# Performance work log

Measured on AMD Instinct MI355X. Metric: run time of the kernel, lower is better.

## Reference

```python
import jax, jax.numpy as jnp
import numpy as np

LOG_STD_MAX = 2.0
LOG_STD_MIN = -5.0
N_LAYERS = 10
HID = 512
OBS = 21
ACT = 8
OVERALL = HID * (N_LAYERS + 1)          # 5632
IN_DIM = OBS + OVERALL                   # 5653
OUT_DIM = OVERALL + ACT                  # 5640
BATCH = 8192


def _block_banded_weight(rng):
    # staircase partitions, exactly as layer_init
    in_d = [0, OBS] + [OBS + HID * i for i in range(1, N_LAYERS + 2)]
    out_d = [0] + [HID * i for i in range(1, N_LAYERS + 2)] + [OUT_DIM]
    W = np.zeros((OUT_DIM, IN_DIM), dtype=np.float32)
    for i in range(N_LAYERS + 2):
        r0, r1 = out_d[i], out_d[i + 1]
        c0, c1 = in_d[i], in_d[i + 1]
        fan_in = c1 - c0
        std = np.sqrt(2.0 / fan_in)  # kaiming_normal_ fan_in, gain sqrt(2)
        W[r0:r1, c0:c1] = rng.standard_normal((r1 - r0, c1 - c0)).astype(np.float32) * std
    return jnp.asarray(W)


def setup_inputs() -> dict:
    key = jax.random.key(0)
    k1, k2, k3, k4, k5, k6 = jax.random.split(key, 6)
    rng = np.random.default_rng(0)
    return {
        "obs": jax.random.normal(k1, (BATCH, OBS), dtype=jnp.float32),
        "hidden0": jax.random.uniform(k2, (BATCH, OVERALL), dtype=jnp.float32),
        "prev_mean": jax.random.normal(k3, (BATCH, ACT), dtype=jnp.float32),
        "prev_logstd": jax.random.normal(k4, (BATCH, ACT), dtype=jnp.float32),
        "W_mean": _block_banded_weight(rng),
        "b_mean": jnp.zeros((OUT_DIM,), dtype=jnp.float32),
        "W_logstd": jax.random.normal(k5, (ACT, IN_DIM), dtype=jnp.float32) / np.sqrt(IN_DIM),
        "b_logstd": jax.random.normal(k6, (ACT,), dtype=jnp.float32) * 0.01,
    }


def reference(obs, hidden0, prev_mean, prev_logstd, W_mean, b_mean, W_logstd, b_logstd):
    x = jnp.concatenate([obs, hidden0], axis=1)            # [B, IN_DIM]
    new_x = x @ W_mean.T + b_mean                          # [B, OUT_DIM]
    new_hidden = jax.nn.relu(new_x[:, :-ACT])              # [B, OVERALL]
    new_mean = new_x[:, -ACT:]                             # [B, ACT]
    new_log_std = x @ W_logstd.T + b_logstd                # [B, ACT]
    # outputs come from the PREVIOUS step's (mean, log_std)
    log_std = jnp.tanh(prev_logstd)
    log_std = LOG_STD_MIN + 0.5 * (LOG_STD_MAX - LOG_STD_MIN) * (log_std + 1.0)
    return (prev_mean, log_std, new_hidden, new_mean, new_log_std)
```

## Files before the change

kernel.cpp:

```cpp
#include <hip/hip_runtime.h>
#include <math.h>

typedef unsigned short u16;
typedef unsigned int u32;
typedef __attribute__((ext_vector_type(8))) short short8;
typedef __attribute__((ext_vector_type(4))) float float4v;

#define BATCH   8192
#define OBS     21
#define HID     512
#define NL      10
#define OVERALL 5632
#define IN_DIM  5653
#define ACT     8

#define O_PM   0
#define O_LS   65536
#define O_NH   131072
#define O_NM   (131072 + BATCH*OVERALL)
#define O_NLS  (O_NM + 65536)

#define WSP_TOTAL (10*512*512)
#define WSP_BYTES ((size_t)WSP_TOTAL * 2)

__device__ __forceinline__ u16 f2bf(float f) {
    u32 u = __float_as_uint(f);
    u32 r = (u + 0x7fffu + ((u >> 16) & 1u)) >> 16;
    return (u16)r;
}
__device__ __forceinline__ u32 pkbf(float a, float b) {
    return (u32)f2bf(a) | ((u32)f2bf(b) << 16);
}
__device__ __forceinline__ void gload_lds16(const void* g, void* l) {
    __builtin_amdgcn_global_load_lds(
        (const __attribute__((address_space(1))) char*)g,
        (__attribute__((address_space(3))) char*)l, 16, 0, 0);
}

__global__ __launch_bounds__(256) void k_pack(const float* __restrict__ Wm,
                                              u16* __restrict__ ws) {
    int idx = blockIdx.x * 256 + threadIdx.x;
    if (idx >= WSP_TOTAL) return;
    int z = idx >> 18;
    int rem = idx & 262143;
    int n = rem >> 9, k = rem & 511;
    float v = Wm[(size_t)(512 * (z + 1) + n) * IN_DIM + OBS + 512 * z + k];
    ws[idx] = f2bf(v);
}

#define BM 128
#define BK 32
#define LDA 40
__global__ __launch_bounds__(1024, 4) void k_fused(
        const float* __restrict__ X,
        const float* __restrict__ Wm_raw,
        const u16* __restrict__ Wp,
        const float* __restrict__ Wls_raw,
        const float* __restrict__ b_mean,
        float* __restrict__ out_h,
        float* __restrict__ out_ls,
        float* __restrict__ out_mean,
        int packed) {
    __shared__ __attribute__((aligned(16))) u16 As[BM * LDA];
    __shared__ __attribute__((aligned(16))) u16 Bs[512 * 32];
    __shared__ __attribute__((aligned(16))) u16 Wt[16 * 520];
    u16* Wt2 = (u16*)Bs;

    int t = threadIdx.x;
    int w = t >> 6, lane = t & 63;
    int quad = lane >> 4, r16 = lane & 15;
    int gm = blockIdx.x * BM;
    int z = blockIdx.y;
    bool mainz = (z < 10);
    int wm = (w >> 3) * 64;
    int wn = (w & 7) * 64;

    {
        int n = t >> 7;
        int k4 = (t & 127) * 4;
        const float* wr = Wls_raw + (size_t)n * IN_DIM + OBS + z * 512 + k4;
        u16* dst = &Wt[n * 520 + k4];
        dst[0] = f2bf(wr[0]); dst[1] = f2bf(wr[1]);
        dst[2] = f2bf(wr[2]); dst[3] = f2bf(wr[3]);
        if (!mainz) {
            const float* wr2 = Wm_raw + (size_t)(OVERALL + n) * IN_DIM + OBS + z * 512 + k4;
            u16* d2 = &Wt2[n * 520 + k4];
            d2[0] = f2bf(wr2[0]); d2[1] = f2bf(wr2[1]);
            d2[2] = f2bf(wr2[2]); d2[3] = f2bf(wr2[3]);
        }
    }

    int arow = t >> 3;
    int acol = (t & 7) * 4;
    const float* gA = X + (size_t)(gm + arow) * OVERALL + (size_t)z * 512 + acol;
    float4 areg = *(const float4*)(gA);

    float4v acc[4][4];
#pragma unroll
    for (int i = 0; i < 4; i++)
#pragma unroll
        for (int j = 0; j < 4; j++) acc[i][j] = (float4v)0.f;
    float4v accL = (float4v)0.f;

    for (int it = 0; it < 16; ++it) {
        int k0 = it * BK;
        __syncthreads();
        {
            uint2 p;
            p.x = pkbf(areg.x, areg.y);
            p.y = pkbf(areg.z, areg.w);
            *(uint2*)&As[arow * LDA + acol] = p;
        }
        if (mainz) {
            if (packed) {
#pragma unroll
                for (int i2 = 0; i2 < 2; ++i2) {
                    int base_row = i2 * 256 + w * 16;
                    int row = base_row + (lane >> 2);
                    int slot = lane & 3;
                    int j = (slot - row) & 3;
                    const u16* g = Wp + (size_t)z * 262144 + (size_t)row * 512 + k0 + j * 8;
                    gload_lds16(g, (char*)Bs + base_row * 64);
                }
            } else {
#pragma unroll
                for (int i2 = 0; i2 < 2; ++i2) {
                    int row = i2 * 256 + w * 16 + (lane >> 2);
                    int slot = lane & 3;
                    int j = (slot - row) & 3;
                    const float* g = Wm_raw + (size_t)(512 * (z + 1) + row) * IN_DIM
                                     + OBS + (size_t)z * 512 + k0 + j * 8;
                    uint4 q;
                    q.x = pkbf(g[0], g[1]); q.y = pkbf(g[2], g[3]);
                    q.z = pkbf(g[4], g[5]); q.w = pkbf(g[6], g[7]);
                    *(uint4*)&Bs[row * 32 + slot * 8] = q;
                }
            }
        }
        __syncthreads();
        if (it < 15) areg = *(const float4*)(gA + (it + 1) * BK);

        if (mainz) {
            short8 bfr[4];
#pragma unroll
            for (int j = 0; j < 4; j++) {
                int n = wn + j * 16 + r16;
                int s = (quad + n) & 3;
                bfr[j] = *(const short8*)&Bs[n * 32 + s * 8];
            }
#pragma unroll
            for (int i2 = 0; i2 < 4; i2++) {
                short8 af = *(const short8*)&As[(wm + i2 * 16 + r16) * LDA + quad * 8];
#pragma unroll
                for (int j = 0; j < 4; j++)
                    acc[i2][j] = __builtin_amdgcn_mfma_f32_16x16x32_bf16(af, bfr[j], acc[i2][j], 0, 0, 0);
            }
        }
        if (w < 8) {
            short8 aL = *(const short8*)&As[(w * 16 + r16) * LDA + quad * 8];
            short8 bL = *(const short8*)&Wt[r16 * 520 + k0 + quad * 8];
            accL = __builtin_amdgcn_mfma_f32_16x16x32_bf16(aL, bL, accL, 0, 0, 0);
        } else if (!mainz) {
            short8 aL = *(const short8*)&As[((w - 8) * 16 + r16) * LDA + quad * 8];
            short8 bL = *(const short8*)&Wt2[r16 * 520 + k0 + quad * 8];
            accL = __builtin_amdgcn_mfma_f32_16x16x32_bf16(aL, bL, accL, 0, 0, 0);
        }
    }

    if (mainz) {
        int colblock = (z + 1) * 512;
#pragma unroll
        for (int j = 0; j < 4; j++) {
            int n_loc = wn + j * 16 + r16;
            float bias = b_mean[colblock + n_loc];
#pragma unroll
            for (int i2 = 0; i2 < 4; i2++) {
                int m0 = gm + wm + i2 * 16 + quad * 4;
#pragma unroll
                for (int r = 0; r < 4; r++) {
                    float v = acc[i2][j][r] + bias;
                    out_h[(size_t)(m0 + r) * OVERALL + colblock + n_loc] = fmaxf(v, 0.f);
                }
            }
        }
    }
    if (w < 8) {
        if (r16 < ACT) {
#pragma unroll
            for (int r = 0; r < 4; r++) {
                int row = gm + w * 16 + quad * 4 + r;
                atomicAdd(&out_ls[(size_t)row * ACT + r16], accL[r]);
            }
        }
    } else if (!mainz) {
        if (r16 < ACT) {
            float bias = b_mean[OVERALL + r16];
#pragma unroll
            for (int r = 0; r < 4; r++) {
                int row = gm + (w - 8) * 16 + quad * 4 + r;
                out_mean[(size_t)row * ACT + r16] = accL[r] + bias;
            }
        }
    }
}

#define B0_ROWS 32
__global__ __launch_bounds__(256) void k_block0(const float* __restrict__ obs,
                                                const float* __restrict__ Wm,
                                                const float* __restrict__ b_mean,
                                                float* __restrict__ out_h) {
    __shared__ float w0[OBS * 512];
    __shared__ float bias_s[512];
    __shared__ float obs_s[B0_ROWS * OBS];
    int t = threadIdx.x;
    int b0 = blockIdx.x * B0_ROWS;
    for (int i = t; i < OBS * 512; i += 256) {
        int n = i / OBS, k = i - n * OBS;
        w0[k * 512 + n] = Wm[(size_t)n * IN_DIM + k];
    }
    for (int i = t; i < 512; i += 256) bias_s[i] = b_mean[i];
    for (int i = t; i < B0_ROWS * OBS; i += 256) obs_s[i] = obs[(size_t)b0 * OBS + i];
    __syncthreads();

    int n0 = (t & 127) * 4;
    int rh = t >> 7;
#pragma unroll 4
    for (int r = 0; r < 16; r++) {
        int row = rh * 16 + r;
        float acc0 = bias_s[n0], acc1 = bias_s[n0 + 1];
        float acc2 = bias_s[n0 + 2], acc3 = bias_s[n0 + 3];
#pragma unroll
        for (int k = 0; k < OBS; k++) {
            float xo = obs_s[row * OBS + k];
            const float* wr = &w0[k * 512 + n0];
            acc0 += xo * wr[0]; acc1 += xo * wr[1];
            acc2 += xo * wr[2]; acc3 += xo * wr[3];
        }
        float4 o;
        o.x = fmaxf(acc0, 0.f); o.y = fmaxf(acc1, 0.f);
        o.z = fmaxf(acc2, 0.f); o.w = fmaxf(acc3, 0.f);
        *(float4*)&out_h[(size_t)(b0 + row) * OVERALL + n0] = o;
    }
}

__global__ __launch_bounds__(256) void k_finish(const float* __restrict__ obs,
                                                const float* __restrict__ Wls,
                                                const float* __restrict__ b_logstd,
                                                const float* __restrict__ pm,
                                                const float* __restrict__ pls,
                                                float* __restrict__ o_pm,
                                                float* __restrict__ o_lstd,
                                                float* __restrict__ o_nls) {
    __shared__ float wobs[ACT * OBS];
    __shared__ float bls[ACT];
    int t = threadIdx.x;
    if (t < ACT * OBS) wobs[t] = Wls[(size_t)(t / OBS) * IN_DIM + (t % OBS)];
    if (t < ACT) bls[t] = b_logstd[t];
    __syncthreads();
    int row = blockIdx.x * 256 + t;
    float ob[OBS];
#pragma unroll
    for (int k = 0; k < OBS; k++) ob[k] = obs[(size_t)row * OBS + k];
#pragma unroll
    for (int n = 0; n < ACT; n++) {
        float a = bls[n];
#pragma unroll
        for (int k = 0; k < OBS; k++) a += ob[k] * wobs[n * OBS + k];
        o_nls[(size_t)row * ACT + n] += a;
    }
    float4 p0 = *(const float4*)(pm + (size_t)row * ACT);
    float4 p1 = *(const float4*)(pm + (size_t)row * ACT + 4);
    *(float4*)(o_pm + (size_t)row * ACT) = p0;
    *(float4*)(o_pm + (size_t)row * ACT + 4) = p1;
    float4 l0 = *(const float4*)(pls + (size_t)row * ACT);
    float4 l1 = *(const float4*)(pls + (size_t)row * ACT + 4);
    float4 q0, q1;
    q0.x = -5.f + 3.5f * (tanhf(l0.x) + 1.f);
    q0.y = -5.f + 3.5f * (tanhf(l0.y) + 1.f);
    q0.z = -5.f + 3.5f * (tanhf(l0.z) + 1.f);
    q0.w = -5.f + 3.5f * (tanhf(l0.w) + 1.f);
    q1.x = -5.f + 3.5f * (tanhf(l1.x) + 1.f);
    q1.y = -5.f + 3.5f * (tanhf(l1.y) + 1.f);
    q1.z = -5.f + 3.5f * (tanhf(l1.z) + 1.f);
    q1.w = -5.f + 3.5f * (tanhf(l1.w) + 1.f);
    *(float4*)(o_lstd + (size_t)row * ACT) = q0;
    *(float4*)(o_lstd + (size_t)row * ACT + 4) = q1;
}

extern "C" void kernel_launch(void* const* d_in, const int* in_sizes, int n_in,
                              void* d_out, int out_size, void* d_ws, size_t ws_size,
                              hipStream_t stream) {
    const float* obs         = (const float*)d_in[0];
    const float* hidden0     = (const float*)d_in[1];
    const float* prev_mean   = (const float*)d_in[2];
    const float* prev_logstd = (const float*)d_in[3];
    const float* W_mean      = (const float*)d_in[4];
    const float* b_mean      = (const float*)d_in[5];
    const float* W_logstd    = (const float*)d_in[6];
    const float* b_logstd    = (const float*)d_in[7];

    float* out   = (float*)d_out;
    float* o_pm  = out + O_PM;
    float* o_ls  = out + O_LS;
    float* o_nh  = out + O_NH;
    float* o_nm  = out + O_NM;
    float* o_nls = out + O_NLS;
    u16*   ws    = (u16*)d_ws;

    int packed = (ws != nullptr && ws_size >= WSP_BYTES) ? 1 : 0;

    if (packed) {
        k_pack<<<(WSP_TOTAL + 255) / 256, 256, 0, stream>>>(W_mean, ws);
    }
    hipMemsetAsync(o_nls, 0, (size_t)BATCH * ACT * sizeof(float), stream);
    k_fused<<<dim3(BATCH / BM, NL + 1), 1024, 0, stream>>>(
        hidden0, W_mean, ws, W_logstd, b_mean, o_nh, o_nls, o_nm, packed);
    k_block0<<<BATCH / B0_ROWS, 256, 0, stream>>>(obs, W_mean, b_mean, o_nh);
    k_finish<<<BATCH / 256, 256, 0, stream>>>(obs, W_logstd, b_logstd,
                                              prev_mean, prev_logstd,
                                              o_pm, o_ls, o_nls);
}
```

Measured before the change: 453.8 us.

## Split fused GEMM blocks into four 256-thread column quarters

Each diagonal block's 512-column output is now split across four smaller workgroups of 256 threads instead of one 1024-thread workgroup, with vectorized 16-wide fp32-to-bf16 conversion for A and the head weights. The goal is more, smaller workgroups for better occupancy and scheduling. The trade-off is that each A tile is read and converted four times, raising global or cache traffic. The B LDS swizzle is also dropped, which may introduce bank conflicts.

```diff
diff --git a/kernel.cpp b/kernel.cpp
--- a/kernel.cpp
+++ b/kernel.cpp
@@ -35,6 +35,19 @@
     __builtin_amdgcn_global_load_lds(
         (const __attribute__((address_space(1))) char*)g,
         (__attribute__((address_space(3))) char*)l, 16, 0, 0);
+}
+__device__ __forceinline__ void cvt16(const float* __restrict__ g, u16* dst) {
+    float4 f0 = *(const float4*)(g);
+    float4 f1 = *(const float4*)(g + 4);
+    float4 f2 = *(const float4*)(g + 8);
+    float4 f3 = *(const float4*)(g + 12);
+    uint4 q0, q1;
+    q0.x = pkbf(f0.x, f0.y); q0.y = pkbf(f0.z, f0.w);
+    q0.z = pkbf(f1.x, f1.y); q0.w = pkbf(f1.z, f1.w);
+    q1.x = pkbf(f2.x, f2.y); q1.y = pkbf(f2.z, f2.w);
+    q1.z = pkbf(f3.x, f3.y); q1.w = pkbf(f3.z, f3.w);
+    *(uint4*)dst = q0;
+    *(uint4*)(dst + 8) = q1;
 }
 
 __global__ __launch_bounds__(256) void k_pack(const float* __restrict__ Wm,
@@ -51,7 +64,7 @@
 #define BM 128
 #define BK 32
 #define LDA 40
-__global__ __launch_bounds__(1024, 4) void k_fused(
+__global__ __launch_bounds__(256, 3) void k_fused(
         const float* __restrict__ X,
         const float* __restrict__ Wm_raw,
         const u16* __restrict__ Wp,
@@ -62,91 +75,97 @@
         float* __restrict__ out_mean,
         int packed) {
     __shared__ __attribute__((aligned(16))) u16 As[BM * LDA];
-    __shared__ __attribute__((aligned(16))) u16 Bs[512 * 32];
-    __shared__ __attribute__((aligned(16))) u16 Wt[16 * 520];
-    u16* Wt2 = (u16*)Bs;
-
-    int t = threadIdx.x;
-    int w = t >> 6, lane = t & 63;
-    int quad = lane >> 4, r16 = lane & 15;
-    int gm = blockIdx.x * BM;
-    int z = blockIdx.y;
-    bool mainz = (z < 10);
-    int wm = (w >> 3) * 64;
-    int wn = (w & 7) * 64;
-
-    {
-        int n = t >> 7;
-        int k4 = (t & 127) * 4;
-        const float* wr = Wls_raw + (size_t)n * IN_DIM + OBS + z * 512 + k4;
-        u16* dst = &Wt[n * 520 + k4];
-        dst[0] = f2bf(wr[0]); dst[1] = f2bf(wr[1]);
-        dst[2] = f2bf(wr[2]); dst[3] = f2bf(wr[3]);
-        if (!mainz) {
-            const float* wr2 = Wm_raw + (size_t)(OVERALL + n) * IN_DIM + OBS + z * 512 + k4;
-            u16* d2 = &Wt2[n * 520 + k4];
-            d2[0] = f2bf(wr2[0]); d2[1] = f2bf(wr2[1]);
-            d2[2] = f2bf(wr2[2]); d2[3] = f2bf(wr2[3]);
-        }
-    }
-
-    int arow = t >> 3;
-    int acol = (t & 7) * 4;
-    const float* gA = X + (size_t)(gm + arow) * OVERALL + (size_t)z * 512 + acol;
-    float4 areg = *(const float4*)(gA);
+    __shared__ __attribute__((aligned(16))) u16 Bs[128 * 32];
+    __shared__ __attribute__((aligned(16))) u16 Wt[8 * 520];
+    __shared__ __attribute__((aligned(16))) u16 Wt2[8 * 520];
+
+    const int t = threadIdx.x;
+    const int w = t >> 6, lane = t & 63;
+    const int quad = lane >> 4, r16 = lane & 15;
+    const int gm = blockIdx.x * BM;
+    const int y = blockIdx.y;
+    const bool mainz = (y < 40);
+    const int z = mainz ? (y >> 2) : 10;
+    const int h = y & 3;
+    const bool do_ls = (!mainz) || (h == 0);
+    const int wm = (w >> 1) * 64;
+    const int wn = (w & 1) * 64;
+
+    if (do_ls) {
+        int n = t >> 5;
+        int k16 = (t & 31) * 16;
+        cvt16(Wls_raw + (size_t)n * IN_DIM + OBS + z * 512 + k16, &Wt[n * 520 + k16]);
+    }
+    if (!mainz) {
+        int n = t >> 5;
+        int k16 = (t & 31) * 16;
+        cvt16(Wm_raw + (size_t)(OVERALL + n) * IN_DIM + OBS + z * 512 + k16,
+              &Wt2[n * 520 + k16]);
+    }
+
+    const int arow = t >> 1;
+    const int ahalf = (t & 1) * 16;
+    const float* gA = X + (size_t)(gm + arow) * OVERALL + (size_t)z * 512 + ahalf;
+    float4 a0 = *(const float4*)(gA);
+    float4 a1 = *(const float4*)(gA + 4);
+    float4 a2 = *(const float4*)(gA + 8);
+    float4 a3 = *(const float4*)(gA + 12);
 
     float4v acc[4][4];
 #pragma unroll
     for (int i = 0; i < 4; i++)
 #pragma unroll
         for (int j = 0; j < 4; j++) acc[i][j] = (float4v)0.f;
-    float4v accL = (float4v)0.f;
+    float4v accL[2], accM[2];
+    accL[0] = (float4v)0.f; accL[1] = (float4v)0.f;
+    accM[0] = (float4v)0.f; accM[1] = (float4v)0.f;
 
     for (int it = 0; it < 16; ++it) {
-        int k0 = it * BK;
+        const int k0 = it * BK;
         __syncthreads();
         {
-            uint2 p;
-            p.x = pkbf(areg.x, areg.y);
-            p.y = pkbf(areg.z, areg.w);
-            *(uint2*)&As[arow * LDA + acol] = p;
+            uint4 qa, qb;
+            qa.x = pkbf(a0.x, a0.y); qa.y = pkbf(a0.z, a0.w);
+            qa.z = pkbf(a1.x, a1.y); qa.w = pkbf(a1.z, a1.w);
+            qb.x = pkbf(a2.x, a2.y); qb.y = pkbf(a2.z, a2.w);
+            qb.z = pkbf(a3.x, a3.y); qb.w = pkbf(a3.z, a3.w);
+            u16* dst = &As[arow * LDA + ahalf];
+            *(uint4*)dst = qa;
+            *(uint4*)(dst + 8) = qb;
         }
         if (mainz) {
             if (packed) {
 #pragma unroll
                 for (int i2 = 0; i2 < 2; ++i2) {
-                    int base_row = i2 * 256 + w * 16;
-                    int row = base_row + (lane >> 2);
-                    int slot = lane & 3;
-                    int j = (slot - row) & 3;
-                    const u16* g = Wp + (size_t)z * 262144 + (size_t)row * 512 + k0 + j * 8;
-                    gload_lds16(g, (char*)Bs + base_row * 64);
+                    int seg = w * 2 + i2;
+                    const u16* g = Wp + (size_t)z * 262144
+                                   + (size_t)(h * 128 + seg * 16 + (lane >> 2)) * 512
+                                   + k0 + (lane & 3) * 8;
+                    gload_lds16(g, (char*)Bs + seg * 1024);
                 }
             } else {
-#pragma unroll
-                for (int i2 = 0; i2 < 2; ++i2) {
-                    int row = i2 * 256 + w * 16 + (lane >> 2);
-                    int slot = lane & 3;
-                    int j = (slot - row) & 3;
-                    const float* g = Wm_raw + (size_t)(512 * (z + 1) + row) * IN_DIM
-                                     + OBS + (size_t)z * 512 + k0 + j * 8;
-                    uint4 q;
-                    q.x = pkbf(g[0], g[1]); q.y = pkbf(g[2], g[3]);
-                    q.z = pkbf(g[4], g[5]); q.w = pkbf(g[6], g[7]);
-                    *(uint4*)&Bs[row * 32 + slot * 8] = q;
-                }
+                int rowi = t >> 1;
+                int half16 = (t & 1) * 16;
+                const float* g = Wm_raw
+                    + (size_t)(512 * (z + 1) + h * 128 + rowi) * IN_DIM
+                    + OBS + (size_t)z * 512 + k0 + half16;
+                cvt16(g, &Bs[rowi * 32 + half16]);
             }
         }
         __syncthreads();
-        if (it < 15) areg = *(const float4*)(gA + (it + 1) * BK);
+        if (it < 15) {
+            a0 = *(const float4*)(gA + (it + 1) * BK);
+            a1 = *(const float4*)(gA + (it + 1) * BK + 4);
+            a2 = *(const float4*)(gA + (it + 1) * BK + 8);
+            a3 = *(const float4*)(gA + (it + 1) * BK + 12);
+        }
 
         if (mainz) {
             short8 bfr[4];
 #pragma unroll
             for (int j = 0; j < 4; j++) {
                 int n = wn + j * 16 + r16;
-                int s = (quad + n) & 3;
-                bfr[j] = *(const short8*)&Bs[n * 32 + s * 8];
+                bfr[j] = *(const short8*)&Bs[n * 32 + quad * 8];
             }
 #pragma unroll
             for (int i2 = 0; i2 < 4; i2++) {
@@ -156,19 +175,22 @@
                     acc[i2][j] = __builtin_amdgcn_mfma_f32_16x16x32_bf16(af, bfr[j], acc[i2][j], 0, 0, 0);
             }
         }
-        if (w < 8) {
-            short8 aL = *(const short8*)&As[(w * 16 + r16) * LDA + quad * 8];
-            short8 bL = *(const short8*)&Wt[r16 * 520 + k0 + quad * 8];
-            accL = __builtin_amdgcn_mfma_f32_16x16x32_bf16(aL, bL, accL, 0, 0, 0);
-        } else if (!mainz) {
-            short8 aL = *(const short8*)&As[((w - 8) * 16 + r16) * LDA + quad * 8];
-            short8 bL = *(const short8*)&Wt2[r16 * 520 + k0 + quad * 8];
-            accL = __builtin_amdgcn_mfma_f32_16x16x32_bf16(aL, bL, accL, 0, 0, 0);
+        if (do_ls) {
+            short8 bL = *(const short8*)&Wt[(r16 & 7) * 520 + k0 + quad * 8];
+            short8 aL0 = *(const short8*)&As[(w * 32 + r16) * LDA + quad * 8];
+            short8 aL1 = *(const short8*)&As[(w * 32 + 16 + r16) * LDA + quad * 8];
+            accL[0] = __builtin_amdgcn_mfma_f32_16x16x32_bf16(aL0, bL, accL[0], 0, 0, 0);
+            accL[1] = __builtin_amdgcn_mfma_f32_16x16x32_bf16(aL1, bL, accL[1], 0, 0, 0);
+            if (!mainz) {
+                short8 bM = *(const short8*)&Wt2[(r16 & 7) * 520 + k0 + quad * 8];
+                accM[0] = __builtin_amdgcn_mfma_f32_16x16x32_bf16(aL0, bM, accM[0], 0, 0, 0);
+                accM[1] = __builtin_amdgcn_mfma_f32_16x16x32_bf16(aL1, bM, accM[1], 0, 0, 0);
+            }
         }
     }
 
     if (mainz) {
-        int colblock = (z + 1) * 512;
+        int colblock = (z + 1) * 512 + h * 128;
 #pragma unroll
         for (int j = 0; j < 4; j++) {
             int n_loc = wn + j * 16 + r16;
@@ -184,23 +206,24 @@
             }
         }
     }
-    if (w < 8) {
-        if (r16 < ACT) {
+    if (do_ls && r16 < ACT) {
+#pragma unroll
+        for (int s = 0; s < 2; ++s)
 #pragma unroll
             for (int r = 0; r < 4; r++) {
-                int row = gm + w * 16 + quad * 4 + r;
-                atomicAdd(&out_ls[(size_t)row * ACT + r16], accL[r]);
-            }
-        }
-    } else if (!mainz) {
-        if (r16 < ACT) {
-            float bias = b_mean[OVERALL + r16];
+                int row = gm + w * 32 + s * 16 + quad * 4 + r;
+                atomicAdd(&out_ls[(size_t)row * ACT + r16], accL[s][r]);
+            }
+    }
+    if (!mainz && r16 < ACT) {
+        float bias = b_mean[OVERALL + r16];
+#pragma unroll
+        for (int s = 0; s < 2; ++s)
 #pragma unroll
             for (int r = 0; r < 4; r++) {
-                int row = gm + (w - 8) * 16 + quad * 4 + r;
-                out_mean[(size_t)row * ACT + r16] = accL[r] + bias;
-            }
-        }
+                int row = gm + w * 32 + s * 16 + quad * 4 + r;
+                out_mean[(size_t)row * ACT + r16] = accM[s][r] + bias;
+            }
     }
 }
 
@@ -313,7 +336,7 @@
         k_pack<<<(WSP_TOTAL + 255) / 256, 256, 0, stream>>>(W_mean, ws);
     }
     hipMemsetAsync(o_nls, 0, (size_t)BATCH * ACT * sizeof(float), stream);
-    k_fused<<<dim3(BATCH / BM, NL + 1), 1024, 0, stream>>>(
+    k_fused<<<dim3(BATCH / BM, 41), 256, 0, stream>>>(
         hidden0, W_mean, ws, W_logstd, b_mean, o_nh, o_nls, o_nm, packed);
     k_block0<<<BATCH / B0_ROWS, 256, 0, stream>>>(obs, W_mean, b_mean, o_nh);
     k_finish<<<BATCH / 256, 256, 0, stream>>>(obs, W_logstd, b_logstd,
```

Result: slower. 474.2 us (+4.5%).
